# Optimization experiments

Hardware: AMD Instinct MI355X
Metric: run time of the kernel (lower is better)

## Reference

```python
import jax, jax.numpy as jnp
import numpy as np

N = 4096   # sequence length (video frames)
M = 1024   # visual feature dim
A = 128    # audio feature dim
EPS = 1e-6


def _layer_norm(x, g, b):
    mu = jnp.mean(x, axis=-1, keepdims=True)
    var = jnp.var(x, axis=-1, keepdims=True)
    return (x - mu) * jax.lax.rsqrt(var + EPS) * g + b


def _self_attention(x, Wk, Wq, Wv, Wo, apperture):
    # x: [n, d]; Linear weights stored torch-style [out, in]
    n = x.shape[0]
    K = x @ Wk.T
    Q = (x @ Wq.T) * 0.06
    V = x @ Wv.T
    logits = Q @ K.T                              # [n, n]
    idx = jnp.arange(n)
    band = jnp.abs(idx[:, None] - idx[None, :]) < apperture  # keep |i-j| < apperture
    logits = jnp.where(band, logits, -jnp.inf)
    att = jax.nn.softmax(logits, axis=-1)
    # torch: y = (V^T @ att)^T == att^T @ V   (note the transpose on att!)
    y = att.T @ V
    return y @ Wo.T, att


def setup_inputs() -> dict:
    key = jax.random.key(0)
    ks = jax.random.split(key, 16)
    s = 0.02
    inp = {
        "x": jax.random.normal(ks[0], (1, N, M), dtype=jnp.float32),
        "audio": jax.random.normal(ks[1], (1, N, A), dtype=jnp.float32),
        # video self-attention (apperture=20)
        "Wk": jax.random.normal(ks[2], (M, M), dtype=jnp.float32) * s,
        "Wq": jax.random.normal(ks[3], (M, M), dtype=jnp.float32) * s,
        "Wv": jax.random.normal(ks[4], (M, M), dtype=jnp.float32) * s,
        "Wo": jax.random.normal(ks[5], (M, M), dtype=jnp.float32) * s,
        # audio self-attention (apperture=40)
        "aWk": jax.random.normal(ks[6], (A, A), dtype=jnp.float32) * s,
        "aWq": jax.random.normal(ks[7], (A, A), dtype=jnp.float32) * s,
        "aWv": jax.random.normal(ks[8], (A, A), dtype=jnp.float32) * s,
        "aWo": jax.random.normal(ks[9], (A, A), dtype=jnp.float32) * s,
        # MLP head
        "ka_w": jax.random.normal(ks[10], (1024, M + A), dtype=jnp.float32) * s,
        "ka_b": jnp.zeros((1024,), dtype=jnp.float32),
        "kd_w": jax.random.normal(ks[11], (1, 1024), dtype=jnp.float32) * s,
        "kd_b": jnp.zeros((1,), dtype=jnp.float32),
        # layer norms (gamma, beta)
        "ln_y_g": jnp.ones((M,), jnp.float32), "ln_y_b": jnp.zeros((M,), jnp.float32),
        "ln_ka_g": jnp.ones((1024,), jnp.float32), "ln_ka_b": jnp.zeros((1024,), jnp.float32),
        "ln_a_g": jnp.ones((A,), jnp.float32), "ln_a_b": jnp.zeros((A,), jnp.float32),
        "ln_a2_g": jnp.ones((A,), jnp.float32), "ln_a2_b": jnp.zeros((A,), jnp.float32),
        "seq_len": N,
        "audio_len": N,
    }
    return inp


def reference(x, audio, Wk, Wq, Wv, Wo, aWk, aWq, aWv, aWo,
              ka_w, ka_b, kd_w, kd_b,
              ln_y_g, ln_y_b, ln_ka_g, ln_ka_b,
              ln_a_g, ln_a_b, ln_a2_g, ln_a2_b,
              seq_len, audio_len):
    m = x.shape[2]
    aud = audio.reshape(audio_len, -1)                 # [n, 128]
    aud = _layer_norm(aud, ln_a2_g, ln_a2_b)
    x2 = x.reshape(-1, m)                              # [n, 1024]

    y, att_weights = _self_attention(x2, Wk, Wq, Wv, Wo, 20)
    aud_y, _ = _self_attention(aud, aWk, aWq, aWv, aWo, 40)

    y = _layer_norm(y + x2, ln_y_g, ln_y_b)            # dropout = identity (eval)
    aud_y = _layer_norm(aud_y + aud, ln_a_g, ln_a_b)

    h = jnp.concatenate([y, aud_y], axis=1)            # [n, 1152]
    h = jax.nn.relu(h @ ka_w.T + ka_b)
    h = _layer_norm(h, ln_ka_g, ln_ka_b)
    out = jax.nn.sigmoid(h @ kd_w.T + kd_b)            # [n, 1]
    return out.reshape(1, -1), att_weights
```

## Files before the change

### kernel.cpp

```cpp
#include <hip/hip_runtime.h>
#include <hip/hip_bf16.h>
#include <math.h>

#define N_SEQ 4096
#define M_DIM 1024
#define A_DIM 128
#define H_DIM 1152

typedef __attribute__((ext_vector_type(4))) float f32x4;
typedef __attribute__((ext_vector_type(8))) short bf16x8;
typedef __attribute__((ext_vector_type(4))) short bf16x4;

__device__ __forceinline__ unsigned short f2b(float f) {
  union { float f; unsigned int u; } v; v.f = f;
  unsigned int u = v.u;
  unsigned int r = (u + 0x7fffu + ((u >> 16) & 1u)) >> 16;
  return (unsigned short)r;
}
__device__ __forceinline__ float b2f(unsigned short u) {
  union { unsigned int i; float f; } v; v.i = ((unsigned int)u) << 16; return v.f;
}
__device__ __forceinline__ void gload_lds16(const void* g, void* l) {
  __builtin_amdgcn_global_load_lds((const __attribute__((address_space(1))) unsigned int*)g,
                                   (__attribute__((address_space(3))) unsigned int*)l,
                                   16, 0, 0);
}

struct CvtArgs {
  const float* src[10];
  unsigned short* dst[10];
  float* zf;
  unsigned int pfx[12];
};
__global__ __launch_bounds__(256) void k_f2b_multi(CvtArgs a) {
  unsigned int g = blockIdx.x * 256 + threadIdx.x;
  if (g >= a.pfx[10]) {
    *reinterpret_cast<float4*>(a.zf + (size_t)(g - a.pfx[10]) * 4) =
        make_float4(0.f, 0.f, 0.f, 0.f);
    return;
  }
  const float* sp = a.src[0];
  unsigned short* dp = a.dst[0];
  unsigned int base = 0;
#pragma unroll
  for (int i = 1; i < 10; i++)
    if (g >= a.pfx[i]) { sp = a.src[i]; dp = a.dst[i]; base = a.pfx[i]; }
  unsigned int i4 = g - base;
  float4 f = *reinterpret_cast<const float4*>(sp + (size_t)i4 * 4);
  ushort4 o;
  o.x = f2b(f.x); o.y = f2b(f.y); o.z = f2b(f.z); o.w = f2b(f.w);
  *reinterpret_cast<ushort4*>(dp + (size_t)i4 * 4) = o;
}

__global__ __launch_bounds__(256) void k_ln(const float* __restrict__ src,
                                            const float* __restrict__ res,
                                            const float* __restrict__ g,
                                            const float* __restrict__ b,
                                            float* __restrict__ dstf,
                                            unsigned short* __restrict__ dstb,
                                            int D, int ostride, int ooff) {
  int i = blockIdx.x, tid = threadIdx.x, wave = tid >> 6, lane = tid & 63;
  __shared__ float rb[8];
  float v[4];
  int cnt = 0;
  float s = 0.f, ss = 0.f;
  for (int t = tid; t < D; t += 256) {
    float x = src[(size_t)i * D + t];
    if (res) x += res[(size_t)i * D + t];
    v[cnt++] = x; s += x; ss += x * x;
  }
  for (int o = 32; o; o >>= 1) { s += __shfl_xor(s, o); ss += __shfl_xor(ss, o); }
  if (!lane) { rb[wave] = s; rb[4 + wave] = ss; }
  __syncthreads();
  float S = rb[0] + rb[1] + rb[2] + rb[3];
  float SS = rb[4] + rb[5] + rb[6] + rb[7];
  float mu = S / (float)D;
  float var = SS / (float)D - mu * mu;
  float rstd = rsqrtf(var + 1e-6f);
  cnt = 0;
  for (int t = tid; t < D; t += 256) {
    float o = (v[cnt++] - mu) * rstd * g[t] + b[t];
    if (dstf) dstf[(size_t)i * D + t] = o;
    if (dstb) dstb[(size_t)i * ostride + ooff + t] = f2b(o);
  }
}

__device__ __forceinline__ void ln_body(const float* __restrict__ src,
                                        const float* __restrict__ res,
                                        const float* __restrict__ g,
                                        const float* __restrict__ b,
                                        unsigned short* __restrict__ dstb,
                                        int D, int ooff, int i, float* rb) {
  int tid = threadIdx.x, wave = tid >> 6, lane = tid & 63;
  float v[4];
  int cnt = 0;
  float s = 0.f, ss = 0.f;
  for (int t = tid; t < D; t += 256) {
    float x = src[(size_t)i * D + t] + res[(size_t)i * D + t];
    v[cnt++] = x; s += x; ss += x * x;
  }
  for (int o = 32; o; o >>= 1) { s += __shfl_xor(s, o); ss += __shfl_xor(ss, o); }
  if (!lane) { rb[wave] = s; rb[4 + wave] = ss; }
  __syncthreads();
  float S = rb[0] + rb[1] + rb[2] + rb[3];
  float SS = rb[4] + rb[5] + rb[6] + rb[7];
  float mu = S / (float)D;
  float var = SS / (float)D - mu * mu;
  float rstd = rsqrtf(var + 1e-6f);
  cnt = 0;
  for (int t = tid; t < D; t += 256) {
    float o = (v[cnt++] - mu) * rstd * g[t] + b[t];
    dstb[(size_t)i * H_DIM + ooff + t] = f2b(o);
  }
}
__global__ __launch_bounds__(256) void k_ln2(const float* __restrict__ s1,
                                             const float* __restrict__ r1,
                                             const float* __restrict__ g1,
                                             const float* __restrict__ b1,
                                             const float* __restrict__ s2,
                                             const float* __restrict__ r2,
                                             const float* __restrict__ g2,
                                             const float* __restrict__ b2,
                                             unsigned short* __restrict__ dstb) {
  __shared__ float rb[8];
  int bid = blockIdx.x;
  if (bid < N_SEQ) ln_body(s1, r1, g1, b1, dstb, 1024, 0, bid, rb);
  else             ln_body(s2, r2, g2, b2, dstb, 128, 1024, bid - N_SEQ, rb);
}

struct GemmDesc {
  const unsigned short* A;
  const unsigned short* B;
  float* Cf;
  unsigned short* Cb;
  int K, N, gx, nb;
};
__global__ __launch_bounds__(256) void k_gemmx(GemmDesc d0, GemmDesc d1) {
  __shared__ __attribute__((aligned(16))) unsigned short As[3][128 * 32];
  __shared__ __attribute__((aligned(16))) unsigned short Bs[3][128 * 32];
  int tid = threadIdx.x;
  int bid = blockIdx.x;
  GemmDesc d = d0;
  int lid = bid;
  if (bid >= d0.nb) { d = d1; lid = bid - d0.nb; }
  int nwg = d.nb, q = nwg >> 3, r = nwg & 7;
  int xcd = lid & 7, idx = lid >> 3;
  int wgid = (xcd < r ? xcd * (q + 1) : r * (q + 1) + (xcd - r) * q) + idx;
  int bx = wgid % d.gx, by = wgid / d.gx;
  int row0 = by * 128, col0 = bx * 128;
  const int K = d.K, N = d.N;

  int wave = tid >> 6, lane = tid & 63;
  int wr = (wave >> 1) * 64, wc = (wave & 1) * 64;
  int lr = lane & 15;
  int lkb = ((((lane >> 4) + ((lr >> 1) & 3)) & 3)) * 16;
  int ch = wave * 2;
  int srow = ch * 16 + (lane >> 2);
  int scol = ((((lane & 3) - ((lane >> 3) & 3)) & 3)) * 8;
  const unsigned short* ga0 = d.A + (size_t)(row0 + srow) * K + scol;
  const unsigned short* ga1 = ga0 + (size_t)16 * K;
  const unsigned short* gb0 = d.B + (size_t)(col0 + srow) * K + scol;
  const unsigned short* gb1 = gb0 + (size_t)16 * K;

  f32x4 acc[4][4];
#pragma unroll
  for (int m = 0; m < 4; m++)
#pragma unroll
    for (int n = 0; n < 4; n++) acc[m][n] = (f32x4){0.f, 0.f, 0.f, 0.f};

  auto STAGE = [&](int buf, int t) {
    int k0 = t << 5;
    char* la = (char*)(&As[buf][0]) + ch * 1024;
    char* lb = (char*)(&Bs[buf][0]) + ch * 1024;
    gload_lds16(ga0 + k0, la);
    gload_lds16(ga1 + k0, la + 1024);
    gload_lds16(gb0 + k0, lb);
    gload_lds16(gb1 + k0, lb + 1024);
  };

  int nt = K >> 5;
  STAGE(0, 0);
  STAGE(1, 1);
  int cur = 0, sb = 2;
  for (int t = 0; t < nt; t++) {
    if (t + 2 < nt) {
      STAGE(sb, t + 2);
      asm volatile("s_waitcnt vmcnt(8)" ::: "memory");
    } else if (t + 1 < nt) {
      asm volatile("s_waitcnt vmcnt(4)" ::: "memory");
    } else {
      asm volatile("s_waitcnt vmcnt(0)" ::: "memory");
    }
    __builtin_amdgcn_s_barrier();
    __builtin_amdgcn_sched_barrier(0);
    const char* pa = (const char*)(&As[cur][0]) + (wr + lr) * 64 + lkb;
    const char* pb = (const char*)(&Bs[cur][0]) + (wc + lr) * 64 + lkb;
    bf16x8 af[4], bfr[4];
#pragma unroll
    for (int m = 0; m < 4; m++) af[m] = *(const bf16x8*)(pa + m * 1024);
#pragma unroll
    for (int n = 0; n < 4; n++) bfr[n] = *(const bf16x8*)(pb + n * 1024);
#pragma unroll
    for (int m = 0; m < 4; m++)
#pragma unroll
      for (int n = 0; n < 4; n++)
        acc[m][n] = __builtin_amdgcn_mfma_f32_16x16x32_bf16(af[m], bfr[n], acc[m][n], 0, 0, 0);
    __builtin_amdgcn_sched_barrier(0);
    __builtin_amdgcn_s_barrier();
    cur = (cur == 2) ? 0 : cur + 1;
    sb = (sb == 2) ? 0 : sb + 1;
  }
  int lq = lane >> 4;
#pragma unroll
  for (int m = 0; m < 4; m++)
#pragma unroll
    for (int n = 0; n < 4; n++)
#pragma unroll
      for (int j = 0; j < 4; j++) {
        int rr = row0 + wr + m * 16 + lq * 4 + j;
        int cc = col0 + wc + n * 16 + lr;
        if (d.Cf) d.Cf[(size_t)rr * N + cc] = acc[m][n][j];
        if (d.Cb) d.Cb[(size_t)rr * N + cc] = f2b(acc[m][n][j]);
      }
}

__global__ __launch_bounds__(256) void k_attn(const unsigned short* __restrict__ kqv,
                                              const unsigned short* __restrict__ akqv,
                                              float* __restrict__ att,
                                              float* __restrict__ P,
                                              float* __restrict__ Pa) {
  __shared__ __attribute__((aligned(16))) char smem[53504];
  int tid = threadIdx.x, wave = tid >> 6, lane = tid & 63;
  if (blockIdx.x < 256) {
    unsigned short(*Qs)[264] = (unsigned short(*)[264])smem;
    unsigned short(*Ks)[264] = (unsigned short(*)[264])(smem + 8448);
    float(*lg)[64] = (float(*)[64])(smem + 42240);
    int i0 = blockIdx.x * 16;
    int jlo = max(i0 - 19, 0);
    int jhi = min(i0 + 34, N_SEQ - 1);
    int nk = jhi - jlo + 1;
    int lr = lane & 15, lke = (lane >> 4) * 8;
    f32x4 acc = (f32x4){0.f, 0.f, 0.f, 0.f};
    for (int kc = 0; kc < M_DIM; kc += 256) {
      __syncthreads();
#pragma unroll
      for (int it = 0; it < 2; it++) {
        int qq = tid + it * 256;
        int rr = qq >> 5, c = (qq & 31) * 8;
        *(bf16x8*)&Qs[rr][c] =
            *(const bf16x8*)&kqv[(size_t)(i0 + rr) * 3072 + 1024 + kc + c];
      }
#pragma unroll
      for (int it = 0; it < 8; it++) {
        int qq = tid + it * 256;
        int rr = qq >> 5, c = (qq & 31) * 8;
        bf16x8 v = {0, 0, 0, 0, 0, 0, 0, 0};
        if (rr < nk) v = *(const bf16x8*)&kqv[(size_t)(jlo + rr) * 3072 + kc + c];
        *(bf16x8*)&Ks[rr][c] = v;
      }
      __syncthreads();
#pragma unroll
      for (int kk = 0; kk < 8; kk++) {
        bf16x8 a = *(const bf16x8*)&Qs[lr][kk * 32 + lke];
        bf16x8 b = *(const bf16x8*)&Ks[wave * 16 + lr][kk * 32 + lke];
        acc = __builtin_amdgcn_mfma_f32_16x16x32_bf16(a, b, acc, 0, 0, 0);
      }
    }
#pragma unroll
    for (int j = 0; j < 4; j++)
      lg[(lane >> 4) * 4 + j][wave * 16 + (lane & 15)] = acc[j] * 0.06f;
    __syncthreads();
#pragma unroll
    for (int qq = 0; qq < 4; qq++) {
      int rr = wave + qq * 4;
      int i = i0 + rr;
      int c = lane;
      int dd = i - (jlo + c);
      bool valid = (c < nk) && (dd > -20) && (dd < 20);
      float v = valid ? lg[rr][c] : -1e30f;
      float mx = v;
      for (int o = 32; o; o >>= 1) mx = fmaxf(mx, __shfl_xor(mx, o));
      float e = valid ? __expf(v - mx) : 0.f;
      float su = e;
      for (int o = 32; o; o >>= 1) su += __shfl_xor(su, o);
      float p = e / su;
      if (valid) {
        att[(size_t)i * N_SEQ + jlo + c] = p;
        P[(size_t)i * 40 + (jlo + c) - max(i - 19, 0)] = p;
      }
    }
  } else {
    unsigned short(*Qs)[136] = (unsigned short(*)[136])smem;
    unsigned short(*Ks)[136] = (unsigned short(*)[136])(smem + 8704);
    float(*lg)[112] = (float(*)[112])(smem + 39168);
    int i0 = (blockIdx.x - 256) * 32;
    int jlo = max(i0 - 39, 0);
    int jhi = min(i0 + 70, N_SEQ - 1);
    int nk = jhi - jlo + 1;
    int lr = lane & 15, lke = (lane >> 4) * 8;
#pragma unroll
    for (int it = 0; it < 2; it++) {
      int qq = tid + it * 256;
      int rr = qq >> 4, c = (qq & 15) * 8;
      *(bf16x8*)&Qs[rr][c] = *(const bf16x8*)&akqv[(size_t)(i0 + rr) * 384 + 128 + c];
    }
#pragma unroll
    for (int it = 0; it < 7; it++) {
      int qq = tid + it * 256;
      int rr = qq >> 4, c = (qq & 15) * 8;
      bf16x8 v = {0, 0, 0, 0, 0, 0, 0, 0};
      if (rr < nk) v = *(const bf16x8*)&akqv[(size_t)(jlo + rr) * 384 + c];
      *(bf16x8*)&Ks[rr][c] = v;
    }
    __syncthreads();
    for (int ff = wave; ff < 14; ff += 4) {
      int fr = ff / 7, fc = ff % 7;
      f32x4 acc = (f32x4){0.f, 0.f, 0.f, 0.f};
#pragma unroll
      for (int kk = 0; kk < 4; kk++) {
        bf16x8 a = *(const bf16x8*)&Qs[fr * 16 + lr][kk * 32 + lke];
        bf16x8 b = *(const bf16x8*)&Ks[fc * 16 + lr][kk * 32 + lke];
        acc = __builtin_amdgcn_mfma_f32_16x16x32_bf16(a, b, acc, 0, 0, 0);
      }
#pragma unroll
      for (int j = 0; j < 4; j++)
        lg[fr * 16 + (lane >> 4) * 4 + j][fc * 16 + (lane & 15)] = acc[j] * 0.06f;
    }
    __syncthreads();
#pragma unroll
    for (int qq = 0; qq < 8; qq++) {
      int rr = wave + qq * 4;
      int i = i0 + rr;
      int c0 = lane, c1 = lane + 64;
      int e0i = i - (jlo + c0), e1i = i - (jlo + c1);
      bool v0 = (c0 < nk) && (e0i > -40) && (e0i < 40);
      bool v1 = (c1 < nk) && (e1i > -40) && (e1i < 40);
      float l0 = v0 ? lg[rr][c0] : -1e30f;
      float l1 = v1 ? lg[rr][min(c1, 111)] : -1e30f;
      float mx = fmaxf(l0, l1);
      for (int o = 32; o; o >>= 1) mx = fmaxf(mx, __shfl_xor(mx, o));
      float e0 = v0 ? __expf(l0 - mx) : 0.f;
      float e1 = v1 ? __expf(l1 - mx) : 0.f;
      float su = e0 + e1;
      for (int o = 32; o; o >>= 1) su += __shfl_xor(su, o);
      float inv = 1.f / su;
      int base = max(i - 39, 0);
      if (v0) Pa[(size_t)i * 79 + (jlo + c0) - base] = e0 * inv;
      if (v1) Pa[(size_t)i * 79 + (jlo + c1) - base] = e1 * inv;
    }
  }
}

__global__ __launch_bounds__(256) void k_pv(const float* __restrict__ P,
                                            const float* __restrict__ Pa,
                                            const unsigned short* __restrict__ kqv,
                                            const unsigned short* __restrict__ akqv,
                                            unsigned short* __restrict__ y0b,
                                            unsigned short* __restrict__ ay0b) {
  int bid = blockIdx.x, tid = threadIdx.x;
  if (bid < 2048) {
    __shared__ float pa_s[2][80];
    int xcd = bid & 7, idx = bid >> 3;
    int half = tid >> 7, d = tid & 127;
    int i = (xcd * 256 + idx) * 2 + half;
    int jlo = max(i - 39, 0), jhi = min(i + 39, N_SEQ - 1);
    int nj = jhi - jlo + 1;
    if (d < nj)
      pa_s[half][d] = Pa[(size_t)(jlo + d) * 79 + (i - max(jlo + d - 39, 0))];
    __syncthreads();
    float acc = 0.f;
#pragma unroll 8
    for (int t = 0; t < 79; t++) {
      bool v = t < nj;
      int j = v ? (jlo + t) : jhi;
      float a = v ? pa_s[half][t] : 0.f;
      acc += a * b2f(akqv[(size_t)j * 384 + 256 + d]);
    }
    ay0b[(size_t)i * 128 + d] = f2b(acc);
  } else {
    __shared__ float pv_s[40];
    int vb = bid - 2048;
    int xcd = vb & 7, idx = vb >> 3;
    int i = xcd * 512 + idx;
    int jlo = max(i - 19, 0), jhi = min(i + 19, N_SEQ - 1);
    int nj = jhi - jlo + 1;
    if (tid < nj)
      pv_s[tid] = P[(size_t)(jlo + tid) * 40 + (i - max(jlo + tid - 19, 0))];
    __syncthreads();
    int d0 = tid * 4;
    float a0 = 0.f, a1 = 0.f, a2 = 0.f, a3 = 0.f;
#pragma unroll
    for (int t = 0; t < 39; t++) {
      bool v = t < nj;
      int j = v ? (jlo + t) : jhi;
      float a = v ? pv_s[t] : 0.f;
      bf16x4 vv = *(const bf16x4*)&kqv[(size_t)j * 3072 + 2048 + d0];
      a0 += a * b2f((unsigned short)vv[0]);
      a1 += a * b2f((unsigned short)vv[1]);
      a2 += a * b2f((unsigned short)vv[2]);
      a3 += a * b2f((unsigned short)vv[3]);
    }
    ushort4 o;
    o.x = f2b(a0); o.y = f2b(a1); o.z = f2b(a2); o.w = f2b(a3);
    *(ushort4*)&y0b[(size_t)i * 1024 + d0] = o;
  }
}

__global__ __launch_bounds__(256) void k_head(const float* __restrict__ h2,
                                              const float* __restrict__ kab,
                                              const float* __restrict__ g,
                                              const float* __restrict__ b,
                                              const float* __restrict__ kdw,
                                              const float* __restrict__ kdb,
                                              float* __restrict__ out) {
  int i = blockIdx.x, tid = threadIdx.x, wave = tid >> 6, lane = tid & 63;
  __shared__ float rb[12];
  float v[4], s = 0.f, ss = 0.f;
#pragma unroll
  for (int q = 0; q < 4; q++) {
    int t = tid + q * 256;
    float x = h2[(size_t)i * 1024 + t] + kab[t];
    x = fmaxf(x, 0.f);
    v[q] = x; s += x; ss += x * x;
  }
  for (int o = 32; o; o >>= 1) { s += __shfl_xor(s, o); ss += __shfl_xor(ss, o); }
  if (!lane) { rb[wave] = s; rb[4 + wave] = ss; }
  __syncthreads();
  float S = rb[0] + rb[1] + rb[2] + rb[3];
  float SS = rb[4] + rb[5] + rb[6] + rb[7];
  float mu = S * (1.f / 1024.f);
  float var = SS * (1.f / 1024.f) - mu * mu;
  float rstd = rsqrtf(var + 1e-6f);
  float dacc = 0.f;
#pragma unroll
  for (int q = 0; q < 4; q++) {
    int t = tid + q * 256;
    dacc += ((v[q] - mu) * rstd * g[t] + b[t]) * kdw[t];
  }
  for (int o = 32; o; o >>= 1) dacc += __shfl_xor(dacc, o);
  if (!lane) rb[8 + wave] = dacc;
  __syncthreads();
  if (tid == 0) out[i] = 1.f / (1.f + __expf(-(rb[8] + rb[9] + rb[10] + rb[11] + kdb[0])));
}

extern "C" void kernel_launch(void* const* d_in, const int* in_sizes, int n_in,
                              void* d_out, int out_size, void* d_ws, size_t ws_size,
                              hipStream_t stream) {
  const float* x      = (const float*)d_in[0];
  const float* audio  = (const float*)d_in[1];
  const float* Wk     = (const float*)d_in[2];
  const float* Wq     = (const float*)d_in[3];
  const float* Wv     = (const float*)d_in[4];
  const float* Wo     = (const float*)d_in[5];
  const float* aWk    = (const float*)d_in[6];
  const float* aWq    = (const float*)d_in[7];
  const float* aWv    = (const float*)d_in[8];
  const float* aWo    = (const float*)d_in[9];
  const float* ka_w   = (const float*)d_in[10];
  const float* ka_b   = (const float*)d_in[11];
  const float* kd_w   = (const float*)d_in[12];
  const float* kd_b   = (const float*)d_in[13];
  const float* ln_y_g = (const float*)d_in[14];
  const float* ln_y_b = (const float*)d_in[15];
  const float* ln_ka_g= (const float*)d_in[16];
  const float* ln_ka_b= (const float*)d_in[17];
  const float* ln_a_g = (const float*)d_in[18];
  const float* ln_a_b = (const float*)d_in[19];
  const float* ln_a2_g= (const float*)d_in[20];
  const float* ln_a2_b= (const float*)d_in[21];

  const size_t MB = 1024ull * 1024ull;
  if (ws_size < 106 * MB) return;

  char* w = (char*)d_ws;
  unsigned short* kqv_bf  = (unsigned short*)(w);
  unsigned short* akqv_bf = (unsigned short*)(w + 24 * MB);
  float* y1    = (float*)(w + 27 * MB);
  float* h2    = (float*)(w + 43 * MB);
  float* aud32 = (float*)(w + 59 * MB);
  float* ay1   = (float*)(w + 61 * MB);
  float* P     = (float*)(w + 63 * MB);
  float* Pa    = (float*)(w + 64 * MB);
  unsigned short* x_bf     = (unsigned short*)(w + 66 * MB);
  unsigned short* wkqv_bf  = (unsigned short*)(w + 74 * MB);
  unsigned short* wo_bf    = (unsigned short*)(w + 80 * MB);
  unsigned short* kaw_bf   = (unsigned short*)(w + 82 * MB);
  unsigned short* awkqv_bf = (unsigned short*)(w + 85 * MB);
  unsigned short* awo_bf   = (unsigned short*)(w + 86 * MB);
  unsigned short* aud_bf   = (unsigned short*)(w + 87 * MB);
  unsigned short* y0_bf    = (unsigned short*)(w + 88 * MB);
  unsigned short* ay0_bf   = (unsigned short*)(w + 96 * MB);
  unsigned short* h_bf     = (unsigned short*)(w + 97 * MB);

  float* out0 = (float*)d_out;
  float* att  = (float*)d_out + N_SEQ;

  CvtArgs ca;
  const unsigned int MM4 = (M_DIM * M_DIM) / 4;
  const unsigned int AA4 = (A_DIM * A_DIM) / 4;
  ca.src[0] = x;    ca.dst[0] = x_bf;
  ca.src[1] = Wk;   ca.dst[1] = wkqv_bf;
  ca.src[2] = Wq;   ca.dst[2] = wkqv_bf + M_DIM * M_DIM;
  ca.src[3] = Wv;   ca.dst[3] = wkqv_bf + 2 * M_DIM * M_DIM;
  ca.src[4] = Wo;   ca.dst[4] = wo_bf;
  ca.src[5] = ka_w; ca.dst[5] = kaw_bf;
  ca.src[6] = aWk;  ca.dst[6] = awkqv_bf;
  ca.src[7] = aWq;  ca.dst[7] = awkqv_bf + A_DIM * A_DIM;
  ca.src[8] = aWv;  ca.dst[8] = awkqv_bf + 2 * A_DIM * A_DIM;
  ca.src[9] = aWo;  ca.dst[9] = awo_bf;
  ca.zf = (float*)d_out;
  unsigned int sz4[10] = { (N_SEQ * M_DIM) / 4, MM4, MM4, MM4, MM4,
                           (1024u * H_DIM) / 4, AA4, AA4, AA4, AA4 };
  ca.pfx[0] = 0;
  for (int i = 0; i < 10; i++) ca.pfx[i + 1] = ca.pfx[i] + sz4[i];
  ca.pfx[11] = ca.pfx[10] + (unsigned int)(out_size / 4);
  k_f2b_multi<<<(ca.pfx[11] + 255) / 256, 256, 0, stream>>>(ca);

  k_ln<<<N_SEQ, 256, 0, stream>>>(audio, nullptr, ln_a2_g, ln_a2_b, aud32, aud_bf,
                                  A_DIM, A_DIM, 0);

  GemmDesc dk { x_bf,   wkqv_bf,  nullptr, kqv_bf,  1024, 3072, 24, 768 };
  GemmDesc da { aud_bf, awkqv_bf, nullptr, akqv_bf, 128,  384,  3,  96  };
  k_gemmx<<<dk.nb + da.nb, 256, 0, stream>>>(dk, da);

  k_attn<<<384, 256, 0, stream>>>(kqv_bf, akqv_bf, att, P, Pa);
  k_pv<<<2048 + N_SEQ, 256, 0, stream>>>(P, Pa, kqv_bf, akqv_bf, y0_bf, ay0_bf);

  GemmDesc dw { y0_bf,  wo_bf,  y1,  nullptr, 1024, 1024, 8, 256 };
  GemmDesc dv { ay0_bf, awo_bf, ay1, nullptr, 128,  128,  1, 32  };
  k_gemmx<<<dw.nb + dv.nb, 256, 0, stream>>>(dw, dv);

  k_ln2<<<2 * N_SEQ, 256, 0, stream>>>(y1, x, ln_y_g, ln_y_b,
                                       ay1, aud32, ln_a_g, ln_a_b, h_bf);

  GemmDesc dm { h_bf, kaw_bf, h2, nullptr, 1152, 1024, 8, 256 };
  GemmDesc dz { nullptr, nullptr, nullptr, nullptr, 32, 128, 1, 0 };
  k_gemmx<<<dm.nb, 256, 0, stream>>>(dm, dz);

  k_head<<<N_SEQ, 256, 0, stream>>>(h2, ka_b, ln_ka_g, ln_ka_b, kd_w, kd_b, out0);
}
```

Before: 179.8 us.

## Store intermediates in bf16, fuse audio LN into convert, zero att in GEMM

The GEMM outputs y1, ay1 and h2 are now written as bf16 instead of fp32, and the layer norms read bf16 inputs, including bf16 residuals (x_bf, aud_bf) in place of fp32 x and aud32. The audio layernorm is folded into the conversion kernel, and zeroing of the attention output moves into extra blocks of the first GEMM launch, which removes one launch. k_ln2 and k_head switch to vectorized loads. This cuts memory traffic and launches at the cost of extra rounding error in the residual and LN paths.

```diff
diff --git a/kernel.cpp b/kernel.cpp
--- a/kernel.cpp
+++ b/kernel.cpp
@@ -29,16 +29,34 @@
 struct CvtArgs {
   const float* src[10];
   unsigned short* dst[10];
-  float* zf;
-  unsigned int pfx[12];
+  unsigned int pfx[11];
+  unsigned int nblk_cvt;
+  const float* audio;
+  const float* lng;
+  const float* lnb;
+  unsigned short* aud_bf;
 };
 __global__ __launch_bounds__(256) void k_f2b_multi(CvtArgs a) {
-  unsigned int g = blockIdx.x * 256 + threadIdx.x;
-  if (g >= a.pfx[10]) {
-    *reinterpret_cast<float4*>(a.zf + (size_t)(g - a.pfx[10]) * 4) =
-        make_float4(0.f, 0.f, 0.f, 0.f);
+  int tid = threadIdx.x;
+  if (blockIdx.x >= a.nblk_cvt) {
+    __shared__ float rb[8];
+    int ab = blockIdx.x - a.nblk_cvt;
+    int i = ab * 2 + (tid >> 7), d = tid & 127;
+    float x = a.audio[(size_t)i * A_DIM + d];
+    float s = x, ss = x * x;
+    for (int o = 32; o; o >>= 1) { s += __shfl_xor(s, o); ss += __shfl_xor(ss, o); }
+    int wave = tid >> 6, lane = tid & 63;
+    if (!lane) { rb[wave] = s; rb[4 + wave] = ss; }
+    __syncthreads();
+    int w0 = (tid >> 7) * 2;
+    float S = rb[w0] + rb[w0 + 1], SS = rb[4 + w0] + rb[4 + w0 + 1];
+    float mu = S * (1.f / 128.f);
+    float var = SS * (1.f / 128.f) - mu * mu;
+    float rstd = rsqrtf(var + 1e-6f);
+    a.aud_bf[(size_t)i * A_DIM + d] = f2b((x - mu) * rstd * a.lng[d] + a.lnb[d]);
     return;
   }
+  unsigned int g = blockIdx.x * 256 + tid;
   const float* sp = a.src[0];
   unsigned short* dp = a.dst[0];
   unsigned int base = 0;
@@ -52,82 +70,6 @@
   *reinterpret_cast<ushort4*>(dp + (size_t)i4 * 4) = o;
 }
 
-__global__ __launch_bounds__(256) void k_ln(const float* __restrict__ src,
-                                            const float* __restrict__ res,
-                                            const float* __restrict__ g,
-                                            const float* __restrict__ b,
-                                            float* __restrict__ dstf,
-                                            unsigned short* __restrict__ dstb,
-                                            int D, int ostride, int ooff) {
-  int i = blockIdx.x, tid = threadIdx.x, wave = tid >> 6, lane = tid & 63;
-  __shared__ float rb[8];
-  float v[4];
-  int cnt = 0;
-  float s = 0.f, ss = 0.f;
-  for (int t = tid; t < D; t += 256) {
-    float x = src[(size_t)i * D + t];
-    if (res) x += res[(size_t)i * D + t];
-    v[cnt++] = x; s += x; ss += x * x;
-  }
-  for (int o = 32; o; o >>= 1) { s += __shfl_xor(s, o); ss += __shfl_xor(ss, o); }
-  if (!lane) { rb[wave] = s; rb[4 + wave] = ss; }
-  __syncthreads();
-  float S = rb[0] + rb[1] + rb[2] + rb[3];
-  float SS = rb[4] + rb[5] + rb[6] + rb[7];
-  float mu = S / (float)D;
-  float var = SS / (float)D - mu * mu;
-  float rstd = rsqrtf(var + 1e-6f);
-  cnt = 0;
-  for (int t = tid; t < D; t += 256) {
-    float o = (v[cnt++] - mu) * rstd * g[t] + b[t];
-    if (dstf) dstf[(size_t)i * D + t] = o;
-    if (dstb) dstb[(size_t)i * ostride + ooff + t] = f2b(o);
-  }
-}
-
-__device__ __forceinline__ void ln_body(const float* __restrict__ src,
-                                        const float* __restrict__ res,
-                                        const float* __restrict__ g,
-                                        const float* __restrict__ b,
-                                        unsigned short* __restrict__ dstb,
-                                        int D, int ooff, int i, float* rb) {
-  int tid = threadIdx.x, wave = tid >> 6, lane = tid & 63;
-  float v[4];
-  int cnt = 0;
-  float s = 0.f, ss = 0.f;
-  for (int t = tid; t < D; t += 256) {
-    float x = src[(size_t)i * D + t] + res[(size_t)i * D + t];
-    v[cnt++] = x; s += x; ss += x * x;
-  }
-  for (int o = 32; o; o >>= 1) { s += __shfl_xor(s, o); ss += __shfl_xor(ss, o); }
-  if (!lane) { rb[wave] = s; rb[4 + wave] = ss; }
-  __syncthreads();
-  float S = rb[0] + rb[1] + rb[2] + rb[3];
-  float SS = rb[4] + rb[5] + rb[6] + rb[7];
-  float mu = S / (float)D;
-  float var = SS / (float)D - mu * mu;
-  float rstd = rsqrtf(var + 1e-6f);
-  cnt = 0;
-  for (int t = tid; t < D; t += 256) {
-    float o = (v[cnt++] - mu) * rstd * g[t] + b[t];
-    dstb[(size_t)i * H_DIM + ooff + t] = f2b(o);
-  }
-}
-__global__ __launch_bounds__(256) void k_ln2(const float* __restrict__ s1,
-                                             const float* __restrict__ r1,
-                                             const float* __restrict__ g1,
-                                             const float* __restrict__ b1,
-                                             const float* __restrict__ s2,
-                                             const float* __restrict__ r2,
-                                             const float* __restrict__ g2,
-                                             const float* __restrict__ b2,
-                                             unsigned short* __restrict__ dstb) {
-  __shared__ float rb[8];
-  int bid = blockIdx.x;
-  if (bid < N_SEQ) ln_body(s1, r1, g1, b1, dstb, 1024, 0, bid, rb);
-  else             ln_body(s2, r2, g2, b2, dstb, 128, 1024, bid - N_SEQ, rb);
-}
-
 struct GemmDesc {
   const unsigned short* A;
   const unsigned short* B;
@@ -135,11 +77,19 @@
   unsigned short* Cb;
   int K, N, gx, nb;
 };
-__global__ __launch_bounds__(256) void k_gemmx(GemmDesc d0, GemmDesc d1) {
+__global__ __launch_bounds__(256) void k_gemmx(GemmDesc d0, GemmDesc d1, float* zf) {
   __shared__ __attribute__((aligned(16))) unsigned short As[3][128 * 32];
   __shared__ __attribute__((aligned(16))) unsigned short Bs[3][128 * 32];
   int tid = threadIdx.x;
   int bid = blockIdx.x;
+  int gemmb = d0.nb + d1.nb;
+  if (bid >= gemmb) {
+    float4* p = (float4*)(zf + (size_t)(bid - gemmb) * 65536);
+    float4 z = make_float4(0.f, 0.f, 0.f, 0.f);
+#pragma unroll
+    for (int k = 0; k < 64; k++) p[tid + k * 256] = z;
+    return;
+  }
   GemmDesc d = d0;
   int lid = bid;
   if (bid >= d0.nb) { d = d1; lid = bid - d0.nb; }
@@ -406,7 +356,62 @@
   }
 }
 
-__global__ __launch_bounds__(256) void k_head(const float* __restrict__ h2,
+__global__ __launch_bounds__(256) void k_ln2(const unsigned short* __restrict__ s1,
+                                             const unsigned short* __restrict__ r1,
+                                             const float* __restrict__ g1,
+                                             const float* __restrict__ b1,
+                                             const unsigned short* __restrict__ s2,
+                                             const unsigned short* __restrict__ r2,
+                                             const float* __restrict__ g2,
+                                             const float* __restrict__ b2,
+                                             unsigned short* __restrict__ dstb) {
+  __shared__ float rb[8];
+  int bid = blockIdx.x, tid = threadIdx.x, wave = tid >> 6, lane = tid & 63;
+  if (bid < N_SEQ) {
+    int i = bid;
+    bf16x4 sv = *(const bf16x4*)&s1[(size_t)i * 1024 + tid * 4];
+    bf16x4 rv = *(const bf16x4*)&r1[(size_t)i * 1024 + tid * 4];
+    float v[4], s = 0.f, ss = 0.f;
+#pragma unroll
+    for (int q = 0; q < 4; q++) {
+      float xx = b2f((unsigned short)sv[q]) + b2f((unsigned short)rv[q]);
+      v[q] = xx; s += xx; ss += xx * xx;
+    }
+    for (int o = 32; o; o >>= 1) { s += __shfl_xor(s, o); ss += __shfl_xor(ss, o); }
+    if (!lane) { rb[wave] = s; rb[4 + wave] = ss; }
+    __syncthreads();
+    float S = rb[0] + rb[1] + rb[2] + rb[3];
+    float SS = rb[4] + rb[5] + rb[6] + rb[7];
+    float mu = S * (1.f / 1024.f);
+    float var = SS * (1.f / 1024.f) - mu * mu;
+    float rstd = rsqrtf(var + 1e-6f);
+    float4 gv = *(const float4*)&g1[tid * 4];
+    float4 bv = *(const float4*)&b1[tid * 4];
+    ushort4 o;
+    o.x = f2b((v[0] - mu) * rstd * gv.x + bv.x);
+    o.y = f2b((v[1] - mu) * rstd * gv.y + bv.y);
+    o.z = f2b((v[2] - mu) * rstd * gv.z + bv.z);
+    o.w = f2b((v[3] - mu) * rstd * gv.w + bv.w);
+    *(ushort4*)&dstb[(size_t)i * H_DIM + tid * 4] = o;
+  } else {
+    int i = bid - N_SEQ;
+    float xx = 0.f;
+    if (tid < 128) xx = b2f(s2[(size_t)i * 128 + tid]) + b2f(r2[(size_t)i * 128 + tid]);
+    float s = xx, ss = xx * xx;
+    for (int o = 32; o; o >>= 1) { s += __shfl_xor(s, o); ss += __shfl_xor(ss, o); }
+    if (!lane) { rb[wave] = s; rb[4 + wave] = ss; }
+    __syncthreads();
+    float S = rb[0] + rb[1] + rb[2] + rb[3];
+    float SS = rb[4] + rb[5] + rb[6] + rb[7];
+    float mu = S * (1.f / 128.f);
+    float var = SS * (1.f / 128.f) - mu * mu;
+    float rstd = rsqrtf(var + 1e-6f);
+    if (tid < 128)
+      dstb[(size_t)i * H_DIM + 1024 + tid] = f2b((xx - mu) * rstd * g2[tid] + b2[tid]);
+  }
+}
+
+__global__ __launch_bounds__(256) void k_head(const unsigned short* __restrict__ h2b,
                                               const float* __restrict__ kab,
                                               const float* __restrict__ g,
                                               const float* __restrict__ b,
@@ -415,14 +420,15 @@
                                               float* __restrict__ out) {
   int i = blockIdx.x, tid = threadIdx.x, wave = tid >> 6, lane = tid & 63;
   __shared__ float rb[12];
+  bf16x4 hv = *(const bf16x4*)&h2b[(size_t)i * 1024 + tid * 4];
+  float4 kb = *(const float4*)&kab[tid * 4];
   float v[4], s = 0.f, ss = 0.f;
-#pragma unroll
-  for (int q = 0; q < 4; q++) {
-    int t = tid + q * 256;
-    float x = h2[(size_t)i * 1024 + t] + kab[t];
-    x = fmaxf(x, 0.f);
-    v[q] = x; s += x; ss += x * x;
-  }
+  v[0] = fmaxf(b2f((unsigned short)hv[0]) + kb.x, 0.f);
+  v[1] = fmaxf(b2f((unsigned short)hv[1]) + kb.y, 0.f);
+  v[2] = fmaxf(b2f((unsigned short)hv[2]) + kb.z, 0.f);
+  v[3] = fmaxf(b2f((unsigned short)hv[3]) + kb.w, 0.f);
+#pragma unroll
+  for (int q = 0; q < 4; q++) { s += v[q]; ss += v[q] * v[q]; }
   for (int o = 32; o; o >>= 1) { s += __shfl_xor(s, o); ss += __shfl_xor(ss, o); }
   if (!lane) { rb[wave] = s; rb[4 + wave] = ss; }
   __syncthreads();
@@ -431,12 +437,13 @@
   float mu = S * (1.f / 1024.f);
   float var = SS * (1.f / 1024.f) - mu * mu;
   float rstd = rsqrtf(var + 1e-6f);
-  float dacc = 0.f;
-#pragma unroll
-  for (int q = 0; q < 4; q++) {
-    int t = tid + q * 256;
-    dacc += ((v[q] - mu) * rstd * g[t] + b[t]) * kdw[t];
-  }
+  float4 gv = *(const float4*)&g[tid * 4];
+  float4 bv = *(const float4*)&b[tid * 4];
+  float4 kv = *(const float4*)&kdw[tid * 4];
+  float dacc = ((v[0] - mu) * rstd * gv.x + bv.x) * kv.x +
+               ((v[1] - mu) * rstd * gv.y + bv.y) * kv.y +
+               ((v[2] - mu) * rstd * gv.z + bv.z) * kv.z +
+               ((v[3] - mu) * rstd * gv.w + bv.w) * kv.w;
   for (int o = 32; o; o >>= 1) dacc += __shfl_xor(dacc, o);
   if (!lane) rb[8 + wave] = dacc;
   __syncthreads();
@@ -470,27 +477,26 @@
   const float* ln_a2_b= (const float*)d_in[21];
 
   const size_t MB = 1024ull * 1024ull;
-  if (ws_size < 106 * MB) return;
+  if (ws_size < 90 * MB) return;
 
   char* w = (char*)d_ws;
   unsigned short* kqv_bf  = (unsigned short*)(w);
   unsigned short* akqv_bf = (unsigned short*)(w + 24 * MB);
-  float* y1    = (float*)(w + 27 * MB);
-  float* h2    = (float*)(w + 43 * MB);
-  float* aud32 = (float*)(w + 59 * MB);
-  float* ay1   = (float*)(w + 61 * MB);
-  float* P     = (float*)(w + 63 * MB);
-  float* Pa    = (float*)(w + 64 * MB);
-  unsigned short* x_bf     = (unsigned short*)(w + 66 * MB);
-  unsigned short* wkqv_bf  = (unsigned short*)(w + 74 * MB);
-  unsigned short* wo_bf    = (unsigned short*)(w + 80 * MB);
-  unsigned short* kaw_bf   = (unsigned short*)(w + 82 * MB);
-  unsigned short* awkqv_bf = (unsigned short*)(w + 85 * MB);
-  unsigned short* awo_bf   = (unsigned short*)(w + 86 * MB);
-  unsigned short* aud_bf   = (unsigned short*)(w + 87 * MB);
-  unsigned short* y0_bf    = (unsigned short*)(w + 88 * MB);
-  unsigned short* ay0_bf   = (unsigned short*)(w + 96 * MB);
-  unsigned short* h_bf     = (unsigned short*)(w + 97 * MB);
+  unsigned short* y1b     = (unsigned short*)(w + 27 * MB);
+  unsigned short* h2b     = (unsigned short*)(w + 35 * MB);
+  unsigned short* ay1b    = (unsigned short*)(w + 43 * MB);
+  float* P     = (float*)(w + 44 * MB);
+  float* Pa    = (float*)(w + 45 * MB);
+  unsigned short* x_bf     = (unsigned short*)(w + 47 * MB);
+  unsigned short* wkqv_bf  = (unsigned short*)(w + 55 * MB);
+  unsigned short* wo_bf    = (unsigned short*)(w + 61 * MB);
+  unsigned short* kaw_bf   = (unsigned short*)(w + 63 * MB);
+  unsigned short* awkqv_bf = (unsigned short*)(w + 66 * MB);
+  unsigned short* awo_bf   = (unsigned short*)(w + 67 * MB);
+  unsigned short* aud_bf   = (unsigned short*)(w + 68 * MB);
+  unsigned short* y0_bf    = (unsigned short*)(w + 69 * MB);
+  unsigned short* ay0_bf   = (unsigned short*)(w + 77 * MB);
+  unsigned short* h_bf     = (unsigned short*)(w + 78 * MB);
 
   float* out0 = (float*)d_out;
   float* att  = (float*)d_out + N_SEQ;
@@ -508,34 +514,31 @@
   ca.src[7] = aWq;  ca.dst[7] = awkqv_bf + A_DIM * A_DIM;
   ca.src[8] = aWv;  ca.dst[8] = awkqv_bf + 2 * A_DIM * A_DIM;
   ca.src[9] = aWo;  ca.dst[9] = awo_bf;
-  ca.zf = (float*)d_out;
   unsigned int sz4[10] = { (N_SEQ * M_DIM) / 4, MM4, MM4, MM4, MM4,
                            (1024u * H_DIM) / 4, AA4, AA4, AA4, AA4 };
   ca.pfx[0] = 0;
   for (int i = 0; i < 10; i++) ca.pfx[i + 1] = ca.pfx[i] + sz4[i];
-  ca.pfx[11] = ca.pfx[10] + (unsigned int)(out_size / 4);
-  k_f2b_multi<<<(ca.pfx[11] + 255) / 256, 256, 0, stream>>>(ca);
-
-  k_ln<<<N_SEQ, 256, 0, stream>>>(audio, nullptr, ln_a2_g, ln_a2_b, aud32, aud_bf,
-                                  A_DIM, A_DIM, 0);
+  ca.nblk_cvt = ca.pfx[10] / 256;
+  ca.audio = audio; ca.lng = ln_a2_g; ca.lnb = ln_a2_b; ca.aud_bf = aud_bf;
+  k_f2b_multi<<<ca.nblk_cvt + 2048, 256, 0, stream>>>(ca);
 
   GemmDesc dk { x_bf,   wkqv_bf,  nullptr, kqv_bf,  1024, 3072, 24, 768 };
   GemmDesc da { aud_bf, awkqv_bf, nullptr, akqv_bf, 128,  384,  3,  96  };
-  k_gemmx<<<dk.nb + da.nb, 256, 0, stream>>>(dk, da);
+  k_gemmx<<<dk.nb + da.nb + 256, 256, 0, stream>>>(dk, da, att);
 
   k_attn<<<384, 256, 0, stream>>>(kqv_bf, akqv_bf, att, P, Pa);
   k_pv<<<2048 + N_SEQ, 256, 0, stream>>>(P, Pa, kqv_bf, akqv_bf, y0_bf, ay0_bf);
 
-  GemmDesc dw { y0_bf,  wo_bf,  y1,  nullptr, 1024, 1024, 8, 256 };
-  GemmDesc dv { ay0_bf, awo_bf, ay1, nullptr, 128,  128,  1, 32  };
-  k_gemmx<<<dw.nb + dv.nb, 256, 0, stream>>>(dw, dv);
-
-  k_ln2<<<2 * N_SEQ, 256, 0, stream>>>(y1, x, ln_y_g, ln_y_b,
-                                       ay1, aud32, ln_a_g, ln_a_b, h_bf);
-
-  GemmDesc dm { h_bf, kaw_bf, h2, nullptr, 1152, 1024, 8, 256 };
+  GemmDesc dw { y0_bf,  wo_bf,  nullptr, y1b,  1024, 1024, 8, 256 };
+  GemmDesc dv { ay0_bf, awo_bf, nullptr, ay1b, 128,  128,  1, 32  };
+  k_gemmx<<<dw.nb + dv.nb, 256, 0, stream>>>(dw, dv, nullptr);
+
+  k_ln2<<<2 * N_SEQ, 256, 0, stream>>>(y1b, x_bf, ln_y_g, ln_y_b,
+                                       ay1b, aud_bf, ln_a_g, ln_a_b, h_bf);
+
+  GemmDesc dm { h_bf, kaw_bf, nullptr, h2b, 1152, 1024, 8, 256 };
   GemmDesc dz { nullptr, nullptr, nullptr, nullptr, 32, 128, 1, 0 };
-  k_gemmx<<<dm.nb, 256, 0, stream>>>(dm, dz);
-
-  k_head<<<N_SEQ, 256, 0, stream>>>(h2, ka_b, ln_ka_g, ln_ka_b, kd_w, kd_b, out0);
-}
+  k_gemmx<<<dm.nb, 256, 0, stream>>>(dm, dz, nullptr);
+
+  k_head<<<N_SEQ, 256, 0, stream>>>(h2b, ka_b, ln_ka_g, ln_ka_b, kd_w, kd_b, out0);
+}
```

Result: faster. 167.9 us (-6.6%).
